# Kernel optimization log

Measured on AMD Instinct MI355X. Metric: run time of the kernel, lower is better.

Reference implementation:

```python
import jax, jax.numpy as jnp
import numpy as np

B, S, D_IN = 2, 2048, 2048
HEADS, HEAD_DIM, N_KV = 32, 64, 8
GROUP = HEADS // N_KV
EPS = 1e-6


def setup_inputs() -> dict:
    key = jax.random.key(0)
    ks = jax.random.split(key, 8)
    x = jax.random.normal(ks[0], (B, S, D_IN), dtype=jnp.float32)
    # causal additive mask: 0 on/below diagonal, -inf above
    mask = jnp.where(jnp.tril(jnp.ones((S, S), dtype=bool)), 0.0, -jnp.inf).astype(jnp.float32)
    # standard RoPE tables over half-dim, tiled to head_dim (rotate-half convention)
    inv_freq = 1.0 / (10000.0 ** (np.arange(0, HEAD_DIM, 2, dtype=np.float32) / HEAD_DIM))
    angles = np.arange(S, dtype=np.float32)[:, None] * inv_freq[None, :]  # [S, D/2]
    angles = np.concatenate([angles, angles], axis=-1)  # [S, D]
    cos = jnp.asarray(np.cos(angles), dtype=jnp.float32)
    sin = jnp.asarray(np.sin(angles), dtype=jnp.float32)
    s = 0.02
    Wq = jax.random.normal(ks[1], (D_IN, HEADS * HEAD_DIM), dtype=jnp.float32) * s
    Wk = jax.random.normal(ks[2], (D_IN, N_KV * HEAD_DIM), dtype=jnp.float32) * s
    Wv = jax.random.normal(ks[3], (D_IN, N_KV * HEAD_DIM), dtype=jnp.float32) * s
    Wo = jax.random.normal(ks[4], (HEADS * HEAD_DIM, D_IN), dtype=jnp.float32) * s
    q_scale = jnp.ones((HEAD_DIM,), dtype=jnp.float32)
    k_scale = jnp.ones((HEAD_DIM,), dtype=jnp.float32)
    return {"x": x, "mask": mask, "cos": cos, "sin": sin,
            "Wq": Wq, "Wk": Wk, "Wv": Wv, "Wo": Wo,
            "q_scale": q_scale, "k_scale": k_scale}


def _rmsnorm(t, w):
    # Qwen3-style RMSNorm over head_dim (computed in fp32)
    var = jnp.mean(jnp.square(t), axis=-1, keepdims=True)
    return (t * jax.lax.rsqrt(var + EPS)) * w


def _rotate_half(t):
    h = t.shape[-1] // 2
    return jnp.concatenate([-t[..., h:], t[..., :h]], axis=-1)


def _rope(t, cos, sin):
    # t: [B, H, S, D]; cos/sin: [S, D]
    return t * cos[None, None, :, :] + _rotate_half(t) * sin[None, None, :, :]


def reference(x, mask, cos, sin, Wq, Wk, Wv, Wo, q_scale, k_scale):
    Bsz, seq, _ = x.shape
    Q = (x @ Wq).reshape(Bsz, seq, HEADS, HEAD_DIM).transpose(0, 2, 1, 3)  # [B,H,S,D]
    K = (x @ Wk).reshape(Bsz, seq, N_KV, HEAD_DIM).transpose(0, 2, 1, 3)   # [B,G,S,D]
    V = (x @ Wv).reshape(Bsz, seq, N_KV, HEAD_DIM).transpose(0, 2, 1, 3)   # [B,G,S,D]
    Q = _rmsnorm(Q, q_scale)
    K = _rmsnorm(K, k_scale)
    Q = _rope(Q, cos[:seq], sin[:seq])
    K = _rope(K, cos[:seq], sin[:seq])
    K = jnp.repeat(K, GROUP, axis=1)  # [B,H,S,D]
    V = jnp.repeat(V, GROUP, axis=1)
    scores = jnp.einsum('bhqd,bhkd->bhqk', Q, K) + mask[:seq, :seq]
    weights = jax.nn.softmax(scores / jnp.sqrt(jnp.float32(HEAD_DIM)), axis=-1)
    vectors = jnp.einsum('bhqk,bhkd->bhqd', weights, V)
    vectors = vectors.transpose(0, 2, 1, 3).reshape(Bsz, seq, HEADS * HEAD_DIM)
    return vectors @ Wo
```

## Files before the change

### kernel.cpp

```cpp
#include <hip/hip_runtime.h>
#include <hip/hip_bf16.h>
#include <stdint.h>

#define S_LEN   2048
#define DIN     2048
#define NHEADS  32
#define HDIM    64
#define NKV     8

typedef __bf16 bf16x8 __attribute__((ext_vector_type(8)));
typedef float  f32x4  __attribute__((ext_vector_type(4)));

#define AS1(p) ((__attribute__((address_space(1))) void*)(void*)(p))
#define AS3(p) ((__attribute__((address_space(3))) void*)(p))
#define MFMA_BF16 __builtin_amdgcn_mfma_f32_16x16x32_bf16

#if __has_builtin(__builtin_amdgcn_exp2f)
#define EXP2F(x) __builtin_amdgcn_exp2f(x)
#else
#define EXP2F(x) exp2f(x)
#endif

static __device__ __forceinline__ unsigned short f2bf(float f) {
  unsigned int x = __float_as_uint(f);
  return (unsigned short)((x + 0x7fffu + ((x >> 16) & 1u)) >> 16);
}
static __device__ __forceinline__ float bf2f(unsigned short u) {
  return __uint_as_float((unsigned int)u << 16);
}

__global__ __launch_bounds__(256) void cast_x_kernel(const float* __restrict__ x,
                                                     unsigned short* __restrict__ xb, int n4) {
  int i = blockIdx.x * 256 + threadIdx.x;
  if (i >= n4) return;
  float4 f = ((const float4*)x)[i];
  ushort4 o = make_ushort4(f2bf(f.x), f2bf(f.y), f2bf(f.z), f2bf(f.w));
  ((ushort4*)xb)[i] = o;
}

__global__ __launch_bounds__(256) void transpose_cast(const float* __restrict__ src,
                                                      unsigned short* __restrict__ dst,
                                                      int K, int N) {
  __shared__ float t[32][33];
  int n0 = blockIdx.x * 32, k0 = blockIdx.y * 32;
  int x = threadIdx.x, y = threadIdx.y;
  #pragma unroll
  for (int j = 0; j < 32; j += 8)
    t[y + j][x] = src[(size_t)(k0 + y + j) * N + n0 + x];
  __syncthreads();
  #pragma unroll
  for (int j = 0; j < 32; j += 8)
    dst[(size_t)(n0 + y + j) * K + k0 + x] = f2bf(t[x][y + j]);
}

__global__ __launch_bounds__(256) void transpose_cast_wqkv(const float* __restrict__ Wq,
                                                           const float* __restrict__ Wk,
                                                           const float* __restrict__ Wv,
                                                           unsigned short* __restrict__ dst) {
  __shared__ float t[32][33];
  int n0 = blockIdx.x * 32, k0 = blockIdx.y * 32;
  const float* src; int col0, srcN;
  if (n0 < 2048)      { src = Wq; col0 = n0;        srcN = 2048; }
  else if (n0 < 2560) { src = Wk; col0 = n0 - 2048; srcN = 512; }
  else                { src = Wv; col0 = n0 - 2560; srcN = 512; }
  int x = threadIdx.x, y = threadIdx.y;
  #pragma unroll
  for (int j = 0; j < 32; j += 8)
    t[y + j][x] = src[(size_t)(k0 + y + j) * srcN + col0 + x];
  __syncthreads();
  #pragma unroll
  for (int j = 0; j < 32; j += 8)
    dst[(size_t)(n0 + y + j) * 2048 + k0 + x] = f2bf(t[x][y + j]);
}

template <typename OutT>
__global__ __launch_bounds__(256) void gemm_nt(const unsigned short* __restrict__ A,
                                               const unsigned short* __restrict__ Bt,
                                               OutT* __restrict__ C,
                                               int M, int N, int K) {
  __shared__ alignas(16) unsigned short As[128 * 32];
  __shared__ alignas(16) unsigned short Bs[128 * 32];
  const int tid = threadIdx.x;
  const int wave = tid >> 6, lane = tid & 63;
  const int g = lane >> 4, c = lane & 15;
  const int m0 = blockIdx.y * 128, n0 = blockIdx.x * 128;
  const int wm = (wave & 1) * 64, wn = (wave >> 1) * 64;

  f32x4 acc[4][4] = {};

  const int ch0 = wave * 2;
  const int p0 = ch0 * 64 + lane, p1 = p0 + 64;
  const int r0 = p0 >> 2, gc0 = ((p0 & 3) ^ ((r0 >> 1) & 3)) * 8;
  const int r1 = p1 >> 2, gc1 = ((p1 & 3) ^ ((r1 >> 1) & 3)) * 8;
  const unsigned short* a0 = A + (size_t)(m0 + r0) * K + gc0;
  const unsigned short* a1 = A + (size_t)(m0 + r1) * K + gc1;
  const unsigned short* b0 = Bt + (size_t)(n0 + r0) * K + gc0;
  const unsigned short* b1 = Bt + (size_t)(n0 + r1) * K + gc1;
  const int fswz = (c >> 1) & 3;

  for (int k0 = 0; k0 < K; k0 += 32) {
    __syncthreads();
    __builtin_amdgcn_global_load_lds(AS1(a0 + k0), AS3(As + ch0 * 512), 16, 0, 0);
    __builtin_amdgcn_global_load_lds(AS1(a1 + k0), AS3(As + ch0 * 512 + 512), 16, 0, 0);
    __builtin_amdgcn_global_load_lds(AS1(b0 + k0), AS3(Bs + ch0 * 512), 16, 0, 0);
    __builtin_amdgcn_global_load_lds(AS1(b1 + k0), AS3(Bs + ch0 * 512 + 512), 16, 0, 0);
    __builtin_amdgcn_s_waitcnt(0);
    __syncthreads();

    bf16x8 af[4], bfr[4];
    #pragma unroll
    for (int i = 0; i < 4; i++)
      af[i] = *(const bf16x8*)(As + (wm + i * 16 + c) * 32 + (g ^ fswz) * 8);
    #pragma unroll
    for (int j = 0; j < 4; j++)
      bfr[j] = *(const bf16x8*)(Bs + (wn + j * 16 + c) * 32 + (g ^ fswz) * 8);
    #pragma unroll
    for (int i = 0; i < 4; i++)
      #pragma unroll
      for (int j = 0; j < 4; j++)
        acc[i][j] = MFMA_BF16(af[i], bfr[j], acc[i][j], 0, 0, 0);
  }

  #pragma unroll
  for (int i = 0; i < 4; i++)
    #pragma unroll
    for (int j = 0; j < 4; j++)
      #pragma unroll
      for (int r = 0; r < 4; r++) {
        size_t idx = (size_t)(m0 + wm + i * 16 + g * 4 + r) * N + n0 + wn + j * 16 + c;
        if constexpr (sizeof(OutT) == 2) C[idx] = f2bf(acc[i][j][r]);
        else                             C[idx] = acc[i][j][r];
      }
}

__global__ __launch_bounds__(256) void norm_rope(const unsigned short* __restrict__ QKV,
                                                 const float* __restrict__ cosb,
                                                 const float* __restrict__ sinb,
                                                 const float* __restrict__ q_scale,
                                                 const float* __restrict__ k_scale,
                                                 unsigned short* __restrict__ Qn,
                                                 unsigned short* __restrict__ Kn) {
  const int tid = threadIdx.x, w = tid >> 6, d = tid & 63;
  const float qs = q_scale[d], ks = k_scale[d];
  #pragma unroll
  for (int k = 0; k < 4; k++) {
    int task = blockIdx.x * 16 + w * 4 + k;
    const int hid = task % 40;
    const int row = task / 40;
    const int b = row >> 11, s = row & 2047;
    float val, sc;
    if (hid < 32) {
      val = bf2f(QKV[(size_t)row * 3072 + hid * 64 + d]);
      sc = qs;
    } else {
      val = bf2f(QKV[(size_t)row * 3072 + 2048 + (hid - 32) * 64 + d]);
      sc = ks;
    }
    float v2 = val * val;
    #pragma unroll
    for (int off = 32; off; off >>= 1) v2 += __shfl_xor(v2, off);
    float t = val * (1.0f / sqrtf(v2 * (1.0f / 64.0f) + 1e-6f)) * sc;
    float partner = __shfl_xor(t, 32);
    float rot = (d < 32) ? -partner : partner;
    float o = t * cosb[s * 64 + d] + rot * sinb[s * 64 + d];
    if (hid < 32) o *= 0.18033688011112042f;
    unsigned short ob = f2bf(o);
    if (hid < 32) Qn[((size_t)(b * 32 + hid) * 2048 + s) * 64 + d] = ob;
    else          Kn[((size_t)(b * 8 + (hid - 32)) * 2048 + s) * 64 + d] = ob;
  }
}

__global__ __launch_bounds__(256) void v_transpose(const unsigned short* __restrict__ QKV,
                                                   unsigned short* __restrict__ Vt) {
  __shared__ unsigned int t[64][65];
  int bid = blockIdx.x;
  const int st = bid & 31, kv = (bid >> 5) & 7, b = bid >> 8;
  const int tid = threadIdx.x, lane = tid & 63, quad = tid >> 6;
  #pragma unroll
  for (int p = 0; p < 16; p++) {
    int sl = p * 4 + quad;
    t[sl][lane] = QKV[(size_t)(b * 2048 + st * 64 + sl) * 3072 + 2560 + kv * 64 + lane];
  }
  __syncthreads();
  size_t base = (size_t)(b * 8 + kv) * 64 * 2048;
  #pragma unroll
  for (int p = 0; p < 16; p++) {
    int dd = p * 4 + quad;
    Vt[base + (size_t)dd * 2048 + st * 64 + lane] = (unsigned short)t[lane][dd];
  }
}

__global__ __launch_bounds__(256, 3) void attn_kernel(const unsigned short* __restrict__ Qn,
                                                      const unsigned short* __restrict__ Kn,
                                                      const unsigned short* __restrict__ Vt,
                                                      unsigned short* __restrict__ Outv) {
  __shared__ alignas(16) unsigned short Ksh[2][4096];
  __shared__ alignas(16) unsigned short Vsh[2][4096];
  __shared__ alignas(16) char Psh[4][4352];

  const int tid = threadIdx.x, w = tid >> 6, lane = tid & 63;
  const int g = lane >> 4, c = lane & 15;
  const int cs = c & 7;
  const int rl = (lane >> 3) & 7;
  const int sl = lane & 7;
  const int swz = (sl ^ rl) << 3;
  const int bid = blockIdx.x;
  const int qt = 63 - (bid >> 4);
  const int rem = bid & 15;
  const int hg = rem & 7, b = rem >> 3;
  const int h = hg * 4 + w;
  const int Q0 = qt * 32;
  const unsigned short* Qp = Qn + ((size_t)(b * NHEADS + h) * S_LEN + Q0) * HDIM;
  const unsigned short* Kp = Kn + (size_t)(b * NKV + hg) * S_LEN * HDIM;
  const unsigned short* Vp = Vt + (size_t)(b * NKV + hg) * HDIM * S_LEN;
  const int ntiles = (qt >> 1) + 1;
  char* PwB = Psh[w];

  bf16x8 bq[2][2];
  #pragma unroll
  for (int iq = 0; iq < 2; iq++)
    #pragma unroll
    for (int t = 0; t < 2; t++)
      bq[iq][t] = *(const bf16x8*)(Qp + (iq * 16 + c) * HDIM + t * 32 + g * 8);

  f32x4 OT[4][2] = {};
  float lv[2] = {0.f, 0.f};

  const int wr0 = w * 16;

  auto STAGE = [&](int kv0s, int bi) {
    #pragma unroll
    for (int q = 0; q < 2; q++) {
      const int rr = wr0 + q * 8;
      __builtin_amdgcn_global_load_lds(AS1(Kp + (size_t)(kv0s + rr + rl) * 64 + swz),
                                       AS3(&Ksh[bi][rr * 64]), 16, 0, 0);
      __builtin_amdgcn_global_load_lds(AS1(Vp + (size_t)(rr + rl) * 2048 + kv0s + swz),
                                       AS3(&Vsh[bi][rr * 64]), 16, 0, 0);
    }
  };

  STAGE(0, 0);
  __syncthreads();

  for (int ti = 0; ti < ntiles; ti++) {
    const int kv0 = ti * 64;
    const int cur = ti & 1;
    if (ti + 1 < ntiles) STAGE(kv0 + 64, cur ^ 1);

    const unsigned short* Kb = Ksh[cur];
    const unsigned short* Vb = Vsh[cur];

    #pragma unroll
    for (int jb = 0; jb < 2; jb++) {
      bf16x8 akx[2][2];
      #pragma unroll
      for (int jt = 0; jt < 2; jt++)
        #pragma unroll
        for (int t = 0; t < 2; t++)
          akx[jt][t] = *(const bf16x8*)(Kb + ((jb * 2 + jt) * 16 + c) * 64 +
                                        (((t * 4 + g) ^ cs) << 3));
      f32x4 Sx[2][2] = {};
      #pragma unroll
      for (int t = 0; t < 2; t++)
        #pragma unroll
        for (int jt = 0; jt < 2; jt++)
          #pragma unroll
          for (int iq = 0; iq < 2; iq++)
            Sx[jt][iq] = MFMA_BF16(akx[jt][t], bq[iq][t], Sx[jt][iq], 0, 0, 0);

      if (ti == ntiles - 1) {
        #pragma unroll
        for (int jt = 0; jt < 2; jt++)
          #pragma unroll
          for (int iq = 0; iq < 2; iq++)
            #pragma unroll
            for (int r = 0; r < 4; r++) {
              int kv = kv0 + (jb * 2 + jt) * 16 + g * 4 + r;
              int q  = Q0 + iq * 16 + c;
              if (kv > q) Sx[jt][iq][r] = -1e30f;
            }
      }

      #pragma unroll
      for (int jt = 0; jt < 2; jt++)
        #pragma unroll
        for (int iq = 0; iq < 2; iq++) {
          f32x4 p;
          #pragma unroll
          for (int r = 0; r < 4; r++) p[r] = EXP2F(Sx[jt][iq][r]);
          lv[iq] += (p[0] + p[1]) + (p[2] + p[3]);
          uint32_t u0 = __float_as_uint(p[0]) + 0x8000u;
          uint32_t u1 = __float_as_uint(p[1]) + 0x8000u;
          uint32_t u2 = __float_as_uint(p[2]) + 0x8000u;
          uint32_t u3 = __float_as_uint(p[3]) + 0x8000u;
          uint32_t lo = __builtin_amdgcn_perm(u1, u0, 0x07060302u);
          uint32_t hi = __builtin_amdgcn_perm(u3, u2, 0x07060302u);
          int row = iq * 16 + c;
          int bytecol = (jb * 2 + jt) * 32 + g * 8;
          uint32_t off = row * 128 + (((bytecol >> 4) ^ (row & 7)) << 4) + (bytecol & 15);
          *(uint2*)(PwB + off) = make_uint2(lo, hi);
        }
    }

    __builtin_amdgcn_s_waitcnt(0xC07F);

    #pragma unroll
    for (int t = 0; t < 2; t++) {
      bf16x8 avt[4];
      #pragma unroll
      for (int dt = 0; dt < 4; dt++)
        avt[dt] = *(const bf16x8*)(Vb + (dt * 16 + c) * 64 + (((t * 4 + g) ^ cs) << 3));
      bf16x8 bpt[2];
      #pragma unroll
      for (int iq = 0; iq < 2; iq++) {
        int row = iq * 16 + c;
        int bytecol = t * 64 + g * 16;
        uint32_t off = row * 128 + (((bytecol >> 4) ^ (row & 7)) << 4);
        bpt[iq] = *(const bf16x8*)(PwB + off);
      }
      #pragma unroll
      for (int dt = 0; dt < 4; dt++)
        #pragma unroll
        for (int iq = 0; iq < 2; iq++)
          OT[dt][iq] = MFMA_BF16(avt[dt], bpt[iq], OT[dt][iq], 0, 0, 0);
    }

    if (ti + 1 < ntiles) __syncthreads();
  }

  float inv[2];
  #pragma unroll
  for (int iq = 0; iq < 2; iq++) {
    float s = lv[iq];
    s += __shfl_xor(s, 16);
    s += __shfl_xor(s, 32);
    inv[iq] = 1.0f / s;
  }

  #pragma unroll
  for (int iq = 0; iq < 2; iq++) {
    const int q = Q0 + iq * 16 + c;
    unsigned short* orow = Outv + (size_t)(b * S_LEN + q) * (NHEADS * HDIM) + h * HDIM;
    #pragma unroll
    for (int dt = 0; dt < 4; dt++) {
      uint32_t u0 = __float_as_uint(OT[dt][iq][0] * inv[iq]) + 0x8000u;
      uint32_t u1 = __float_as_uint(OT[dt][iq][1] * inv[iq]) + 0x8000u;
      uint32_t u2 = __float_as_uint(OT[dt][iq][2] * inv[iq]) + 0x8000u;
      uint32_t u3 = __float_as_uint(OT[dt][iq][3] * inv[iq]) + 0x8000u;
      uint32_t lo = __builtin_amdgcn_perm(u1, u0, 0x07060302u);
      uint32_t hi = __builtin_amdgcn_perm(u3, u2, 0x07060302u);
      *(uint2*)(orow + dt * 16 + g * 4) = make_uint2(lo, hi);
    }
  }
}

extern "C" void kernel_launch(void* const* d_in, const int* in_sizes, int n_in,
                              void* d_out, int out_size, void* d_ws, size_t ws_size,
                              hipStream_t stream) {
  const float* x       = (const float*)d_in[0];
  const float* cosb    = (const float*)d_in[2];
  const float* sinb    = (const float*)d_in[3];
  const float* Wq      = (const float*)d_in[4];
  const float* Wk      = (const float*)d_in[5];
  const float* Wv      = (const float*)d_in[6];
  const float* Wo      = (const float*)d_in[7];
  const float* q_scale = (const float*)d_in[8];
  const float* k_scale = (const float*)d_in[9];

  char* ws = (char*)d_ws;
  unsigned short* xb   = (unsigned short*)(ws);
  unsigned short* wcat = (unsigned short*)(ws + (16ull << 20));
  unsigned short* wo_t = (unsigned short*)(ws + (28ull << 20));
  unsigned short* qkv  = (unsigned short*)(ws + (36ull << 20));
  unsigned short* qn   = (unsigned short*)(ws + (84ull << 20));
  unsigned short* kn   = (unsigned short*)(ws + (100ull << 20));
  unsigned short* vt   = (unsigned short*)(ws + (104ull << 20));
  unsigned short* vec  = (unsigned short*)(ws + (36ull << 20));

  cast_x_kernel<<<8192, 256, 0, stream>>>(x, xb, 2097152);
  dim3 tb(32, 8);
  transpose_cast_wqkv<<<dim3(96, 64), tb, 0, stream>>>(Wq, Wk, Wv, wcat);
  transpose_cast<<<dim3(64, 64), tb, 0, stream>>>(Wo, wo_t, 2048, 2048);

  gemm_nt<unsigned short><<<dim3(24, 32), 256, 0, stream>>>(xb, wcat, qkv, 4096, 3072, 2048);
  norm_rope<<<10240, 256, 0, stream>>>(qkv, cosb, sinb, q_scale, k_scale, qn, kn);
  v_transpose<<<512, 256, 0, stream>>>(qkv, vt);
  attn_kernel<<<1024, 256, 0, stream>>>(qn, kn, vt, vec);
  gemm_nt<float><<<dim3(16, 32), 256, 0, stream>>>(vec, wo_t, (float*)d_out, 4096, 2048, 2048);
}
```

Measured before the change: 340.0 us.

## Replace QKV GEMM with 256x256-tile four-stage LDS ring pipeline

Adds a dedicated QKV projection GEMM that uses 256x256 output tiles with 512 threads per block. A four-buffer LDS ring, filled by direct global-to-LDS loads, keeps three K-steps in flight, with vmcnt-based waits and one barrier per step. The larger tile raises reuse per loaded byte and the deeper prefetch is meant to hide global latency behind MFMA work. The cost is 128KB of LDS and a large accumulator per thread. The grid also shrinks to 192 blocks, which may underfill the 256 CUs.

```diff
diff --git a/kernel.cpp b/kernel.cpp
--- a/kernel.cpp
+++ b/kernel.cpp
@@ -130,6 +130,81 @@
         size_t idx = (size_t)(m0 + wm + i * 16 + g * 4 + r) * N + n0 + wn + j * 16 + c;
         if constexpr (sizeof(OutT) == 2) C[idx] = f2bf(acc[i][j][r]);
         else                             C[idx] = acc[i][j][r];
+      }
+}
+
+__global__ __launch_bounds__(512, 2) void gemm_qkv_ring(const unsigned short* __restrict__ A,
+                                                        const unsigned short* __restrict__ Bt,
+                                                        unsigned short* __restrict__ C) {
+  constexpr int K = 2048, N = 3072, NT = 64;
+  __shared__ alignas(16) unsigned short As[4][8192];
+  __shared__ alignas(16) unsigned short Bs[4][8192];
+  const int tid = threadIdx.x;
+  const int wave = tid >> 6, lane = tid & 63;
+  const int g = lane >> 4, c = lane & 15;
+  const int m0 = blockIdx.y * 256, n0 = blockIdx.x * 256;
+  const int wr = wave >> 2, wc = wave & 3;
+
+  const unsigned short* sA[2];
+  const unsigned short* sB[2];
+  #pragma unroll
+  for (int ch = 0; ch < 2; ch++) {
+    int P = ch * 8192 + tid * 16;
+    int L = P ^ (((P >> 6) & 3) << 4);
+    int r = L >> 6, cw = (L & 63) >> 1;
+    sA[ch] = A + (size_t)(m0 + r) * K + cw;
+    sB[ch] = Bt + (size_t)(n0 + r) * K + cw;
+  }
+
+  const int swzr = (g * 16) ^ ((c & 3) << 4);
+  const int baseA = ((wr * 128 + c) * 64 + swzr) >> 1;
+  const int baseB = ((wc * 64 + c) * 64 + swzr) >> 1;
+
+  f32x4 acc[8][4] = {};
+
+  auto STAGE = [&](int t) {
+    const int s = t & 3;
+    const int ko = t * 32;
+    #pragma unroll
+    for (int ch = 0; ch < 2; ch++) {
+      __builtin_amdgcn_global_load_lds(AS1(sA[ch] + ko), AS3(&As[s][ch * 4096 + wave * 512]), 16, 0, 0);
+      __builtin_amdgcn_global_load_lds(AS1(sB[ch] + ko), AS3(&Bs[s][ch * 4096 + wave * 512]), 16, 0, 0);
+    }
+  };
+
+  STAGE(0); STAGE(1); STAGE(2);
+  asm volatile("s_waitcnt vmcnt(8)" ::: "memory");
+  __builtin_amdgcn_s_barrier();
+
+  for (int t = 0; t < NT; t++) {
+    if (t + 3 < NT) STAGE(t + 3);
+    const int s = t & 3;
+    bf16x8 af[8], bf[4];
+    #pragma unroll
+    for (int i = 0; i < 8; i++) af[i] = *(const bf16x8*)(&As[s][baseA + i * 512]);
+    #pragma unroll
+    for (int j = 0; j < 4; j++) bf[j] = *(const bf16x8*)(&Bs[s][baseB + j * 512]);
+    __builtin_amdgcn_s_setprio(1);
+    #pragma unroll
+    for (int i = 0; i < 8; i++)
+      #pragma unroll
+      for (int j = 0; j < 4; j++)
+        acc[i][j] = MFMA_BF16(af[i], bf[j], acc[i][j], 0, 0, 0);
+    __builtin_amdgcn_s_setprio(0);
+    if (t + 3 < NT)      asm volatile("s_waitcnt vmcnt(8)" ::: "memory");
+    else if (t + 2 < NT) asm volatile("s_waitcnt vmcnt(4)" ::: "memory");
+    else                 asm volatile("s_waitcnt vmcnt(0)" ::: "memory");
+    __builtin_amdgcn_s_barrier();
+  }
+
+  #pragma unroll
+  for (int i = 0; i < 8; i++)
+    #pragma unroll
+    for (int j = 0; j < 4; j++)
+      #pragma unroll
+      for (int r = 0; r < 4; r++) {
+        size_t idx = (size_t)(m0 + wr * 128 + i * 16 + g * 4 + r) * N + n0 + wc * 64 + j * 16 + c;
+        C[idx] = f2bf(acc[i][j][r]);
       }
 }
 
@@ -382,7 +457,7 @@
   transpose_cast_wqkv<<<dim3(96, 64), tb, 0, stream>>>(Wq, Wk, Wv, wcat);
   transpose_cast<<<dim3(64, 64), tb, 0, stream>>>(Wo, wo_t, 2048, 2048);
 
-  gemm_nt<unsigned short><<<dim3(24, 32), 256, 0, stream>>>(xb, wcat, qkv, 4096, 3072, 2048);
+  gemm_qkv_ring<<<dim3(12, 16), 512, 0, stream>>>(xb, wcat, qkv);
   norm_rope<<<10240, 256, 0, stream>>>(qkv, cosb, sinb, q_scale, k_scale, qn, kn);
   v_transpose<<<512, 256, 0, stream>>>(qkv, vt);
   attn_kernel<<<1024, 256, 0, stream>>>(qn, kn, vt, vec);
```

After: 355.3 us. 4.5% more time.

## Pipeline GEMM global-to-LDS loads with a four-stage ring buffer

Applied to the files above, without the earlier changes.

Replaces the single-buffered GEMM main loop with a 4-slot LDS ring that prefetches three K-tiles ahead using direct global-to-LDS loads. Partial vmcnt waits replace full drains, and one barrier per iteration replaces two. MFMA sections run under raised wave priority. This aims to hide global-load latency behind matrix math, at the cost of 64 KB of LDS per block, which lowers occupancy.

```diff
diff --git a/kernel.cpp b/kernel.cpp
--- a/kernel.cpp
+++ b/kernel.cpp
@@ -74,12 +74,12 @@
 }
 
 template <typename OutT>
-__global__ __launch_bounds__(256) void gemm_nt(const unsigned short* __restrict__ A,
-                                               const unsigned short* __restrict__ Bt,
-                                               OutT* __restrict__ C,
-                                               int M, int N, int K) {
-  __shared__ alignas(16) unsigned short As[128 * 32];
-  __shared__ alignas(16) unsigned short Bs[128 * 32];
+__global__ __launch_bounds__(256) void gemm_ring(const unsigned short* __restrict__ A,
+                                                 const unsigned short* __restrict__ Bt,
+                                                 OutT* __restrict__ C,
+                                                 int M, int N, int K) {
+  __shared__ alignas(16) unsigned short As[4][4096];
+  __shared__ alignas(16) unsigned short Bs[4][4096];
   const int tid = threadIdx.x;
   const int wave = tid >> 6, lane = tid & 63;
   const int g = lane >> 4, c = lane & 15;
@@ -98,27 +98,42 @@
   const unsigned short* b1 = Bt + (size_t)(n0 + r1) * K + gc1;
   const int fswz = (c >> 1) & 3;
 
-  for (int k0 = 0; k0 < K; k0 += 32) {
-    __syncthreads();
-    __builtin_amdgcn_global_load_lds(AS1(a0 + k0), AS3(As + ch0 * 512), 16, 0, 0);
-    __builtin_amdgcn_global_load_lds(AS1(a1 + k0), AS3(As + ch0 * 512 + 512), 16, 0, 0);
-    __builtin_amdgcn_global_load_lds(AS1(b0 + k0), AS3(Bs + ch0 * 512), 16, 0, 0);
-    __builtin_amdgcn_global_load_lds(AS1(b1 + k0), AS3(Bs + ch0 * 512 + 512), 16, 0, 0);
-    __builtin_amdgcn_s_waitcnt(0);
-    __syncthreads();
-
+  const int NT = K >> 5;
+
+  auto STAGE = [&](int t) {
+    const int s = t & 3;
+    const int ko = t * 32;
+    __builtin_amdgcn_global_load_lds(AS1(a0 + ko), AS3(&As[s][ch0 * 512]), 16, 0, 0);
+    __builtin_amdgcn_global_load_lds(AS1(a1 + ko), AS3(&As[s][ch0 * 512 + 512]), 16, 0, 0);
+    __builtin_amdgcn_global_load_lds(AS1(b0 + ko), AS3(&Bs[s][ch0 * 512]), 16, 0, 0);
+    __builtin_amdgcn_global_load_lds(AS1(b1 + ko), AS3(&Bs[s][ch0 * 512 + 512]), 16, 0, 0);
+  };
+
+  STAGE(0); STAGE(1); STAGE(2);
+  asm volatile("s_waitcnt vmcnt(8)" ::: "memory");
+  __builtin_amdgcn_s_barrier();
+
+  for (int t = 0; t < NT; t++) {
+    if (t + 3 < NT) STAGE(t + 3);
+    const int s = t & 3;
     bf16x8 af[4], bfr[4];
     #pragma unroll
     for (int i = 0; i < 4; i++)
-      af[i] = *(const bf16x8*)(As + (wm + i * 16 + c) * 32 + (g ^ fswz) * 8);
+      af[i] = *(const bf16x8*)(&As[s][(wm + i * 16 + c) * 32 + (g ^ fswz) * 8]);
     #pragma unroll
     for (int j = 0; j < 4; j++)
-      bfr[j] = *(const bf16x8*)(Bs + (wn + j * 16 + c) * 32 + (g ^ fswz) * 8);
+      bfr[j] = *(const bf16x8*)(&Bs[s][(wn + j * 16 + c) * 32 + (g ^ fswz) * 8]);
+    __builtin_amdgcn_s_setprio(1);
     #pragma unroll
     for (int i = 0; i < 4; i++)
       #pragma unroll
       for (int j = 0; j < 4; j++)
         acc[i][j] = MFMA_BF16(af[i], bfr[j], acc[i][j], 0, 0, 0);
+    __builtin_amdgcn_s_setprio(0);
+    if (t + 3 < NT)      asm volatile("s_waitcnt vmcnt(8)" ::: "memory");
+    else if (t + 2 < NT) asm volatile("s_waitcnt vmcnt(4)" ::: "memory");
+    else                 asm volatile("s_waitcnt vmcnt(0)" ::: "memory");
+    __builtin_amdgcn_s_barrier();
   }
 
   #pragma unroll
@@ -382,9 +397,9 @@
   transpose_cast_wqkv<<<dim3(96, 64), tb, 0, stream>>>(Wq, Wk, Wv, wcat);
   transpose_cast<<<dim3(64, 64), tb, 0, stream>>>(Wo, wo_t, 2048, 2048);
 
-  gemm_nt<unsigned short><<<dim3(24, 32), 256, 0, stream>>>(xb, wcat, qkv, 4096, 3072, 2048);
+  gemm_ring<unsigned short><<<dim3(24, 32), 256, 0, stream>>>(xb, wcat, qkv, 4096, 3072, 2048);
   norm_rope<<<10240, 256, 0, stream>>>(qkv, cosb, sinb, q_scale, k_scale, qn, kn);
   v_transpose<<<512, 256, 0, stream>>>(qkv, vt);
   attn_kernel<<<1024, 256, 0, stream>>>(qn, kn, vt, vec);
-  gemm_nt<float><<<dim3(16, 32), 256, 0, stream>>>(vec, wo_t, (float*)d_out, 4096, 2048, 2048);
-}
+  gemm_ring<float><<<dim3(16, 32), 256, 0, stream>>>(vec, wo_t, (float*)d_out, 4096, 2048, 2048);
+}
```

Result: slower. 353.3 us (+3.9%).
